# Kernel tuning notes

Measured on AMD Instinct MI355X. Metric: run time of the kernel, lower is better.

The kernel has to match this reference:

```python
import jax, jax.numpy as jnp
import numpy as np

GAMMA, ZETA = -0.1, 1.1
N_BITS = 4
QMAX = (1 << N_BITS) - 1  # 15
OUT, IN, D, K = 4096, 4096, 8, 4096
L = (OUT * IN) // D  # 2097152 blocks, no padding needed


def setup_inputs() -> dict:
    key = jax.random.key(0)
    k = jax.random.split(key, 7)
    x = jax.random.normal(k[0], (4, 2048, IN), jnp.float32)
    codebook = jax.random.normal(k[1], (K, D), jnp.float32)
    indices = jax.random.randint(k[2], (L,), 0, K, jnp.int32)
    base_int = jax.random.randint(k[3], (OUT, IN), 0, QMAX, jnp.int32)
    scale = jax.random.uniform(k[4], (OUT, 1), jnp.float32)
    zero = jax.random.uniform(k[5], (OUT, 1), jnp.float32)
    bias = jax.random.normal(k[6], (OUT,), jnp.float32)
    return {"x": x, "codebook": codebook, "indices": indices,
            "base_int": base_int, "scale": scale, "zero": zero, "bias": bias}


def reference(x, codebook, indices, base_int, scale, zero, bias):
    # Gather codebook blocks and rebuild alpha with the weight's shape [OUT, IN]
    alpha = codebook[indices].reshape(OUT, IN)
    # Rectified sigmoid (soft quant mode)
    r = jnp.clip(jax.nn.sigmoid(alpha) * (ZETA - GAMMA) + GAMMA, 0.0, 1.0)
    # Affine int-quant reconstruction
    q_int = jnp.clip(base_int.astype(scale.dtype) + r + zero, 0.0, float(QMAX))
    Wq = scale * (q_int - zero)  # [OUT, IN]
    # F.linear: x @ Wq^T + bias
    return jnp.einsum('bsi,oi->bso', x, Wq) + bias
```

## Files before the change

### kernel.cpp

```cpp
#include <hip/hip_runtime.h>

#define M_DIM 8192
#define N_DIM 4096
#define K_DIM 4096
#define L_BLK 2097152
#define K2 8192

typedef __attribute__((ext_vector_type(8))) short short8;
typedef __attribute__((ext_vector_type(8))) unsigned short ushort8;
typedef __attribute__((ext_vector_type(4))) float f32x4;

__device__ __forceinline__ unsigned short f2bf(float f) {
  unsigned int u = __float_as_uint(f);
  unsigned int r = (u + 0x7fffu + ((u >> 16) & 1u)) >> 16;
  return (unsigned short)r;
}

__device__ __forceinline__ void gld16(const void* g, void* l) {
  __builtin_amdgcn_global_load_lds(
      (const __attribute__((address_space(1))) void*)g,
      (__attribute__((address_space(3))) void*)l, 16, 0, 0);
}

__global__ void prep_kernel(const float* __restrict__ cb,
                            const int* __restrict__ idx,
                            const int* __restrict__ base,
                            const float* __restrict__ scale,
                            const float* __restrict__ zero,
                            const float* __restrict__ x,
                            unsigned short* __restrict__ W,
                            unsigned short* __restrict__ xb) {
  if (blockIdx.x < L_BLK / 256) {
    const int b = blockIdx.x * 256 + threadIdx.x;
    const int o = b >> 9;
    const float s = scale[o];
    const float z = zero[o];
    const int ci = idx[b];
    const float4* crow = (const float4*)(cb + (size_t)ci * 8);
    float4 c0 = crow[0], c1 = crow[1];
    const int4* brow = (const int4*)(base + (size_t)b * 8);
    int4 b0 = brow[0], b1 = brow[1];
    float a[8]  = {c0.x, c0.y, c0.z, c0.w, c1.x, c1.y, c1.z, c1.w};
    int   bi[8] = {b0.x, b0.y, b0.z, b0.w, b1.x, b1.y, b1.z, b1.w};
    union { unsigned short h[8]; ushort8 v; } u;
#pragma unroll
    for (int d = 0; d < 8; ++d) {
      float sg = 1.0f / (1.0f + __expf(-a[d]));
      float r = fminf(fmaxf(sg * 1.2f - 0.1f, 0.0f), 1.0f);
      float q = fminf(fmaxf((float)bi[d] + r + z, 0.0f), 15.0f);
      u.h[d] = f2bf(s * (q - z));
    }
    *(ushort8*)(W + (size_t)b * 8) = u.v;
  } else {
    const size_t i = (size_t)(blockIdx.x - L_BLK / 256) * 256 + threadIdx.x;
    const float4* X = (const float4*)x;
    float4 a0 = X[i * 2], a1 = X[i * 2 + 1];
    float f[8] = {a0.x, a0.y, a0.z, a0.w, a1.x, a1.y, a1.z, a1.w};
    union { unsigned short h[8]; ushort8 v; } u;
#pragma unroll
    for (int d = 0; d < 8; ++d) u.h[d] = f2bf(f[d]);
    *(ushort8*)(xb + i * 8) = u.v;
  }
}


#define VMW(N) asm volatile("s_waitcnt vmcnt(" #N ")" ::: "memory")
#define BAR __builtin_amdgcn_s_barrier()

#define RDB(BF, BUFO) \
  _Pragma("unroll") for (int n = 0; n < 4; ++n) \
  _Pragma("unroll") for (int kk = 0; kk < 2; ++kk) \
    BF[n][kk] = *(const short8*)(lds + (BUFO) + 32768 + \
        (wn * 64 + n * 16 + r16) * 128 + (acol0 ^ (kk << 6)));

#define RDA(AF, BUFO, P) \
  _Pragma("unroll") for (int mi = 0; mi < 2; ++mi) \
  _Pragma("unroll") for (int kk = 0; kk < 2; ++kk) \
    AF[mi][kk] = *(const short8*)(lds + (BUFO) + \
        (wm * 128 + (2 * (P) + mi) * 16 + r16) * 128 + (acol0 ^ (kk << 6)));

#define FMQ(P, AF, BF) do { \
  __builtin_amdgcn_s_setprio(1); \
  _Pragma("unroll") for (int kk = 0; kk < 2; ++kk) \
  _Pragma("unroll") for (int mi = 0; mi < 2; ++mi) \
  _Pragma("unroll") for (int n = 0; n < 4; ++n) \
    acc[2 * (P) + mi][n] = __builtin_amdgcn_mfma_f32_16x16x32_bf16( \
        AF[mi][kk], BF[n][kk], acc[2 * (P) + mi][n], 0, 0, 0); \
  __builtin_amdgcn_s_setprio(0); \
} while (0)

#define ITER(CUR, NXT, T) do { \
   RDA(afA, CUR, 0); RDB(bf, CUR); \
  stA(NXT, 1, (T) + 1); stA(NXT, 3, (T) + 1); \
  BAR; FMQ(0, afA, bf); BAR; \
   RDA(afB, CUR, 1); \
  stB(CUR, 0, (T) + 2); stB(CUR, 1, (T) + 2); \
  BAR; FMQ(1, afB, bf); BAR; \
   RDA(afA, CUR, 2); \
  stB(CUR, 2, (T) + 2); stB(CUR, 3, (T) + 2); \
  BAR; FMQ(2, afA, bf); BAR; \
   RDA(afB, CUR, 3); \
  stA(CUR, 0, (T) + 2); stA(CUR, 2, (T) + 2); \
  VMW(6); BAR; FMQ(3, afB, bf); BAR; \
} while (0)

__global__ __launch_bounds__(512, 2)
void gemm_bt(const unsigned short* __restrict__ A,
             const unsigned short* __restrict__ B,
             const float* __restrict__ bias,
             float* __restrict__ C) {
  __shared__ char lds[131072];
  const int tid = threadIdx.x;
  const int lane = tid & 63;
  const int w = tid >> 6;
  const int wm = w >> 2;
  const int wn = w & 3;
  const int r16 = lane & 15;
  const int g = lane >> 4;
  const int acol0 = (g << 4) ^ ((r16 & 7) << 4);

  const int s = (int)blockIdx.x;
  const int wg = (s & 7) * 64 + (s >> 3);
  const int bm = wg & 31;
  const int bn = wg >> 5;

  const char* Abase = (const char*)A + (size_t)bm * 256 * K2;
  const char* Bbase = (const char*)B + (size_t)bn * 256 * K2;

  const int strow = tid >> 3;
  const int scol = ((tid & 7) * 16) ^ ((strow & 7) << 4);
  const int sdst = w * 1024;

  auto stA = [&](int bo, int c, int kt) {
    gld16(Abase + (size_t)(c * 64 + strow) * K2 + kt * 128 + scol,
          lds + bo + c * 8192 + sdst);
  };
  auto stB = [&](int bo, int c, int kt) {
    gld16(Bbase + (size_t)(c * 64 + strow) * K2 + kt * 128 + scol,
          lds + bo + 32768 + c * 8192 + sdst);
  };

  f32x4 acc[8][4] = {};
  short8 bf[4][2];
  short8 afA[2][2], afB[2][2];

  stB(0, 0, 0); stB(0, 1, 0); stB(0, 2, 0); stB(0, 3, 0);
  stA(0, 0, 0); stA(0, 1, 0); stA(0, 2, 0); stA(0, 3, 0);
  stB(65536, 0, 1); stB(65536, 1, 1); stB(65536, 2, 1); stB(65536, 3, 1);
  stA(65536, 0, 1); stA(65536, 2, 1);
  VMW(6); BAR;

  for (int tp = 0; tp < 31; ++tp) {
    ITER(0, 65536, 2 * tp);
    ITER(65536, 0, 2 * tp + 1);
  }
  RDA(afA, 0, 0); RDB(bf, 0);
  stA(65536, 1, 63); stA(65536, 3, 63);
  BAR; FMQ(0, afA, bf); BAR;
  RDA(afB, 0, 1);
  BAR; FMQ(1, afB, bf); BAR;
  RDA(afA, 0, 2);
  BAR; FMQ(2, afA, bf); BAR;
  RDA(afB, 0, 3);
  VMW(0); BAR; FMQ(3, afB, bf); BAR;
  RDA(afA, 65536, 0); RDB(bf, 65536);
  FMQ(0, afA, bf);
  RDA(afB, 65536, 1);
  FMQ(1, afB, bf);
  RDA(afA, 65536, 2);
  FMQ(2, afA, bf);
  RDA(afB, 65536, 3);
  FMQ(3, afB, bf);

  const int cb0 = bn * 256 + wn * 64 + r16;
  float bv[4];
#pragma unroll
  for (int n = 0; n < 4; ++n) bv[n] = bias[cb0 + n * 16];
#pragma unroll
  for (int m = 0; m < 8; ++m) {
#pragma unroll
    for (int j = 0; j < 4; ++j) {
      int row = bm * 256 + wm * 128 + m * 16 + g * 4 + j;
      float* Crow = C + (size_t)row * N_DIM + cb0;
#pragma unroll
      for (int n = 0; n < 4; ++n) Crow[n * 16] = acc[m][n][j] + bv[n];
    }
  }
}

extern "C" void kernel_launch(void* const* d_in, const int* in_sizes, int n_in,
                              void* d_out, int out_size, void* d_ws, size_t ws_size,
                              hipStream_t stream) {
  const float* x     = (const float*)d_in[0];
  const float* cb    = (const float*)d_in[1];
  const int*   idx   = (const int*)d_in[2];
  const int*   base  = (const int*)d_in[3];
  const float* scale = (const float*)d_in[4];
  const float* zero  = (const float*)d_in[5];
  const float* bias  = (const float*)d_in[6];
  float* out = (float*)d_out;

  unsigned short* Wq = (unsigned short*)d_ws;
  unsigned short* Xb = (unsigned short*)((char*)d_ws + (size_t)N_DIM * K_DIM * 2);

  const int prep_blocks = L_BLK / 256 + (M_DIM * K_DIM / 8) / 256;
  prep_kernel<<<prep_blocks, 256, 0, stream>>>(cb, idx, base, scale, zero, x, Wq, Xb);
  gemm_bt<<<(M_DIM / 256) * (N_DIM / 256), 512, 0, stream>>>(Xb, Wq, bias, out);
}
```

Before: 307.0 us.

## Software-pipeline LDS fragment reads one MFMA phase ahead with double-buffered B registers

After: 302.7 us. No clear change (-1.4%).

```diff
diff --git a/kernel.cpp b/kernel.cpp
--- a/kernel.cpp
+++ b/kernel.cpp
@@ -89,19 +89,24 @@
   __builtin_amdgcn_s_setprio(0); \
 } while (0)
 
-#define ITER(CUR, NXT, T) do { \
-   RDA(afA, CUR, 0); RDB(bf, CUR); \
+#define ITER(BFC, BFN, CUR, NXT, T) do { \
+   \
   stA(NXT, 1, (T) + 1); stA(NXT, 3, (T) + 1); \
-  BAR; FMQ(0, afA, bf); BAR; \
-   RDA(afB, CUR, 1); \
+  RDA(afB, CUR, 1); \
+  BAR; FMQ(0, afA, BFC); BAR; \
+   \
   stB(CUR, 0, (T) + 2); stB(CUR, 1, (T) + 2); \
-  BAR; FMQ(1, afB, bf); BAR; \
-   RDA(afA, CUR, 2); \
+  RDA(afA, CUR, 2); \
+  BAR; FMQ(1, afB, BFC); BAR; \
+   \
   stB(CUR, 2, (T) + 2); stB(CUR, 3, (T) + 2); \
-  BAR; FMQ(2, afA, bf); BAR; \
-   RDA(afB, CUR, 3); \
+  RDA(afB, CUR, 3); \
+  BAR; FMQ(2, afA, BFC); BAR; \
+   \
   stA(CUR, 0, (T) + 2); stA(CUR, 2, (T) + 2); \
-  VMW(6); BAR; FMQ(3, afB, bf); BAR; \
+  VMW(6); BAR; \
+  RDB(BFN, NXT); RDA(afA, NXT, 0); \
+  FMQ(3, afB, BFC); BAR; \
 } while (0)
 
 __global__ __launch_bounds__(512, 2)
@@ -141,7 +146,7 @@
   };
 
   f32x4 acc[8][4] = {};
-  short8 bf[4][2];
+  short8 bfA[4][2], bfB[4][2];
   short8 afA[2][2], afB[2][2];
 
   stB(0, 0, 0); stB(0, 1, 0); stB(0, 2, 0); stB(0, 3, 0);
@@ -149,28 +154,29 @@
   stB(65536, 0, 1); stB(65536, 1, 1); stB(65536, 2, 1); stB(65536, 3, 1);
   stA(65536, 0, 1); stA(65536, 2, 1);
   VMW(6); BAR;
+  RDB(bfA, 0); RDA(afA, 0, 0);
 
   for (int tp = 0; tp < 31; ++tp) {
-    ITER(0, 65536, 2 * tp);
-    ITER(65536, 0, 2 * tp + 1);
+    ITER(bfA, bfB, 0, 65536, 2 * tp);
+    ITER(bfB, bfA, 65536, 0, 2 * tp + 1);
   }
-  RDA(afA, 0, 0); RDB(bf, 0);
   stA(65536, 1, 63); stA(65536, 3, 63);
-  BAR; FMQ(0, afA, bf); BAR;
   RDA(afB, 0, 1);
-  BAR; FMQ(1, afB, bf); BAR;
+  BAR; FMQ(0, afA, bfA); BAR;
   RDA(afA, 0, 2);
-  BAR; FMQ(2, afA, bf); BAR;
+  BAR; FMQ(1, afB, bfA); BAR;
   RDA(afB, 0, 3);
-  VMW(0); BAR; FMQ(3, afB, bf); BAR;
-  RDA(afA, 65536, 0); RDB(bf, 65536);
-  FMQ(0, afA, bf);
+  BAR; FMQ(2, afA, bfA); BAR;
+  VMW(0); BAR;
+  RDB(bfB, 65536); RDA(afA, 65536, 0);
+  FMQ(3, afB, bfA); BAR;
   RDA(afB, 65536, 1);
-  FMQ(1, afB, bf);
+  FMQ(0, afA, bfB);
   RDA(afA, 65536, 2);
-  FMQ(2, afA, bf);
+  FMQ(1, afB, bfB);
   RDA(afB, 65536, 3);
-  FMQ(3, afB, bf);
+  FMQ(2, afA, bfB);
+  FMQ(3, afB, bfB);
 
   const int cb0 = bn * 256 + wn * 64 + r16;
   float bv[4];
```
